# Performance work log

Hardware: AMD Instinct MI355X
Metric: run time of the kernel (lower is better)

The kernel has to match this reference:

```python
import jax, jax.numpy as jnp
import numpy as np

B, N, F_IN, H, S = 8, 2048, 128, 128, 2
ALPHA = 0.1  # LeakyReLU slope


def setup_inputs() -> dict:
    key = jax.random.key(0)
    ks = jax.random.split(key, 10)
    X_bt = jax.random.normal(ks[0], (B, N, F_IN), dtype=jnp.float32)
    distance_matrix = jax.random.uniform(ks[1], (N, N), dtype=jnp.float32)
    sigmas = jnp.array([0.2, 1.0], dtype=jnp.float32)  # GaussianKernelGenerator scales[:2]
    # Per-scale GeoGATLayer params (stacked on leading scale dim)
    W_w = jax.random.normal(ks[2], (S, H, F_IN), dtype=jnp.float32) * (1.0 / np.sqrt(F_IN))
    W_b = jnp.zeros((S, H), dtype=jnp.float32)
    # attn_fc: Linear(2H, 1) split into the two halves acting on h_i and h_j
    a_i = jax.random.normal(ks[3], (S, H), dtype=jnp.float32) * (1.0 / np.sqrt(2 * H))
    a_j = jax.random.normal(ks[4], (S, H), dtype=jnp.float32) * (1.0 / np.sqrt(2 * H))
    a_b = jnp.zeros((S,), dtype=jnp.float32)
    thr = jnp.full((S,), 0.3, dtype=jnp.float32)
    fus_w = jax.random.normal(ks[5], (H, S * H), dtype=jnp.float32) * (1.0 / np.sqrt(S * H))
    fus_b = jnp.zeros((H,), dtype=jnp.float32)
    return {"X_bt": X_bt, "distance_matrix": distance_matrix, "sigmas": sigmas,
            "W_w": W_w, "W_b": W_b, "a_i": a_i, "a_j": a_j, "a_b": a_b,
            "thr": thr, "fus_w": fus_w, "fus_b": fus_b}


def _leaky_relu(x):
    return jnp.where(x >= 0, x, ALPHA * x)


def reference(X_bt, distance_matrix, sigmas, W_w, W_b, a_i, a_j, a_b, thr, fus_w, fus_b):
    n = distance_matrix.shape[0]
    # layer clones dist and sets diag=1.0 (only for the 1/d additive bias)
    dist_diag1 = distance_matrix.at[jnp.diag_indices(n)].set(1.0)
    inv_d = 1.0 / (dist_diag1 + 1e-5)  # (N,N)
    outs = []
    for s in range(S):
        h = jnp.einsum('bnf,hf->bnh', X_bt, W_w[s]) + W_b[s]  # (B,N,H)
        # attn_fc(cat(h_i,h_j)) == h_i@a_i + h_j@a_j + bias (no concat materialized)
        si = h @ a_i[s]  # (B,N)
        sj = h @ a_j[s]  # (B,N)
        e = _leaky_relu(si[:, :, None] + sj[:, None, :] + a_b[s])  # (B,N,N)
        e = e + inv_d[None]
        A = jnp.exp(-distance_matrix ** 2 / (2.0 * sigmas[s] ** 2))  # Gaussian kernel
        mask = jax.nn.sigmoid(10.0 * (A - thr[s]))
        e = e * mask[None]
        attn = jax.nn.softmax(e, axis=-1)  # dropout is identity in eval
        outs.append(jnp.einsum('bnm,bmh->bnh', attn, h))
    H_cat = jnp.concatenate(outs, axis=-1)  # (B,N,S*H)
    return jnp.einsum('bnk,hk->bnh', H_cat, fus_w) + fus_b
```

## Files before the change

### kernel.cpp

```cpp
#include <hip/hip_runtime.h>
#include <cstdint>
#include <cstddef>

#define BB 8
#define NN 2048
#define FF 128
#define HH 128
#define SS 2
#define NT (NN / 64)

typedef _Float16 f16x8 __attribute__((ext_vector_type(8)));
typedef _Float16 f16x4 __attribute__((ext_vector_type(4)));
typedef float f32x4 __attribute__((ext_vector_type(4)));

__global__ __launch_bounds__(256) void geo_kernel(
    const float* __restrict__ dist, const float* __restrict__ sigmas,
    const float* __restrict__ thr, _Float16* __restrict__ g1, float* __restrict__ g2)
{
    const size_t idx = ((size_t)blockIdx.x * 256 + threadIdx.x) * 8;
    const int s = (int)(idx >> 22);
    const int i = (int)((idx >> 11) & (NN - 1));
    const int j0 = (int)(idx & (NN - 1));
    const float sg = sigmas[s];
    const float inv2s2 = 1.0f / (2.0f * sg * sg);
    const float th = thr[s];
    const float* dp = dist + (size_t)i * NN + j0;
    float4 d0 = *(const float4*)dp, d1 = *(const float4*)(dp + 4);
    float dv[8] = {d0.x, d0.y, d0.z, d0.w, d1.x, d1.y, d1.z, d1.w};
    f16x8 o1; float og[8];
    #pragma unroll
    for (int k = 0; k < 8; ++k) {
        float d = dv[k];
        float A = __expf(-d * d * inv2s2);
        float msk = 1.0f / (1.0f + __expf(-10.0f * (A - th)));
        float dd = (j0 + k == i) ? 1.0f : d;
        float invd = 1.0f / (dd + 1e-5f);
        o1[k] = (_Float16)msk;
        og[k] = msk * invd;
    }
    *(f16x8*)(g1 + idx) = o1;
    *(float4*)(g2 + idx)     = (float4){og[0], og[1], og[2], og[3]};
    *(float4*)(g2 + idx + 4) = (float4){og[4], og[5], og[6], og[7]};
}

__global__ __launch_bounds__(256, 2) void prep_kernel(
    const float* __restrict__ X, const float* __restrict__ Ww, const float* __restrict__ Wb,
    const float* __restrict__ ai, const float* __restrict__ aj, const float* __restrict__ ab,
    _Float16* __restrict__ h_t, float* __restrict__ srow, float* __restrict__ scol)
{
    const int s = blockIdx.z, b = blockIdx.y;
    const int n0 = blockIdx.x * 64;
    const int tid = threadIdx.x;
    __shared__ __align__(16) unsigned char smem[51200];
    float* sredI = (float*)(smem + 49152);
    float* sredJ = (float*)(smem + 49152 + 1024);

    {
        const int r = tid >> 2, fq = tid & 3;
        const float* src = X + ((size_t)b * NN + n0 + r) * FF + fq * 32;
        unsigned char* dst = smem + r * 256;
        const unsigned rs = r & 15;
        #pragma unroll
        for (int k = 0; k < 4; ++k) {
            float4 v0 = *(const float4*)(src + k * 8);
            float4 v1 = *(const float4*)(src + k * 8 + 4);
            f16x8 h;
            h[0]=(_Float16)v0.x; h[1]=(_Float16)v0.y; h[2]=(_Float16)v0.z; h[3]=(_Float16)v0.w;
            h[4]=(_Float16)v1.x; h[5]=(_Float16)v1.y; h[6]=(_Float16)v1.z; h[7]=(_Float16)v1.w;
            *(f16x8*)(dst + (((fq * 4 + k) ^ rs) << 4)) = h;
        }
    }
    {
        const int ch = tid >> 1, kh8 = (tid & 1) * 8;
        const float* src = Ww + ((size_t)s * HH + ch) * FF + kh8 * 8;
        unsigned char* dst = smem + 16384 + ch * 256;
        const unsigned cs = ch & 15;
        #pragma unroll
        for (int k = 0; k < 8; ++k) {
            float4 v0 = *(const float4*)(src + k * 8);
            float4 v1 = *(const float4*)(src + k * 8 + 4);
            f16x8 h;
            h[0]=(_Float16)v0.x; h[1]=(_Float16)v0.y; h[2]=(_Float16)v0.z; h[3]=(_Float16)v0.w;
            h[4]=(_Float16)v1.x; h[5]=(_Float16)v1.y; h[6]=(_Float16)v1.z; h[7]=(_Float16)v1.w;
            *(f16x8*)(dst + (((kh8 + k) ^ cs) << 4)) = h;
        }
    }
    __syncthreads();

    const int wave = tid >> 6, lane = tid & 63;
    const int lm = lane & 15, lq = lane >> 4;
    f32x4 acc[4][2];
    #pragma unroll
    for (int m = 0; m < 4; ++m)
        #pragma unroll
        for (int n = 0; n < 2; ++n) acc[m][n] = (f32x4){0.f, 0.f, 0.f, 0.f};

    #pragma unroll
    for (int ks = 0; ks < 4; ++ks) {
        f16x8 af[4], bf[2];
        #pragma unroll
        for (int m = 0; m < 4; ++m) {
            int r = m * 16 + lm;
            af[m] = *(const f16x8*)(smem + r * 256 + ((((ks << 2) | lq) ^ (r & 15)) << 4));
        }
        #pragma unroll
        for (int n = 0; n < 2; ++n) {
            int ch = wave * 32 + n * 16 + lm;
            bf[n] = *(const f16x8*)(smem + 16384 + ch * 256 + ((((ks << 2) | lq) ^ (ch & 15)) << 4));
        }
        #pragma unroll
        for (int m = 0; m < 4; ++m)
            #pragma unroll
            for (int n = 0; n < 2; ++n)
                acc[m][n] = __builtin_amdgcn_mfma_f32_16x16x32_f16(af[m], bf[n], acc[m][n], 0, 0, 0);
    }

    const float wb0 = Wb[s * HH + wave * 32 + lm];
    const float wb1 = Wb[s * HH + wave * 32 + 16 + lm];
    const float ai0 = ai[s * HH + wave * 32 + lm];
    const float ai1 = ai[s * HH + wave * 32 + 16 + lm];
    const float aj0 = aj[s * HH + wave * 32 + lm];
    const float aj1 = aj[s * HH + wave * 32 + 16 + lm];
    float pI[4][4], pJ[4][4];
    #pragma unroll
    for (int m = 0; m < 4; ++m) {
        #pragma unroll
        for (int r = 0; r < 4; ++r) {
            float h0 = acc[m][0][r] + wb0;
            float h1 = acc[m][1][r] + wb1;
            pI[m][r] = h0 * ai0 + h1 * ai1;
            pJ[m][r] = h0 * aj0 + h1 * aj1;
        }
        #pragma unroll
        for (int n = 0; n < 2; ++n) {
            float wb = n ? wb1 : wb0;
            f16x4 hv;
            #pragma unroll
            for (int r = 0; r < 4; ++r) hv[r] = (_Float16)(acc[m][n][r] + wb);
            int ch = wave * 32 + n * 16 + lm;
            *(f16x4*)(h_t + ((size_t)((s * BB + b) * HH + ch)) * NN + n0 + m * 16 + lq * 4) = hv;
        }
    }
    #pragma unroll
    for (int st = 1; st < 16; st <<= 1) {
        #pragma unroll
        for (int m = 0; m < 4; ++m)
            #pragma unroll
            for (int r = 0; r < 4; ++r) {
                pI[m][r] += __shfl_xor(pI[m][r], st);
                pJ[m][r] += __shfl_xor(pJ[m][r], st);
            }
    }
    if (lm == 0) {
        #pragma unroll
        for (int m = 0; m < 4; ++m)
            #pragma unroll
            for (int r = 0; r < 4; ++r) {
                sredI[wave * 64 + m * 16 + lq * 4 + r] = pI[m][r];
                sredJ[wave * 64 + m * 16 + lq * 4 + r] = pJ[m][r];
            }
    }
    __syncthreads();
    if (tid < 64) {
        float sI = sredI[tid] + sredI[64 + tid] + sredI[128 + tid] + sredI[192 + tid] + ab[s];
        float sJ = sredJ[tid] + sredJ[64 + tid] + sredJ[128 + tid] + sredJ[192 + tid];
        size_t idx = (size_t)(s * BB + b) * NN + n0 + tid;
        srow[idx] = sI;
        scol[idx] = sJ;
    }
}

template<bool GEO>
__global__ __launch_bounds__(256, 3) void attn_kernel(
    const float* __restrict__ dist, const float* __restrict__ sigmas,
    const float* __restrict__ thr, const _Float16* __restrict__ h_t,
    const float* __restrict__ srow, const float* __restrict__ scol,
    const _Float16* __restrict__ g1, const float* __restrict__ g2,
    _Float16* __restrict__ Hcat)
{
    const int s = blockIdx.z, b = blockIdx.y;
    const int i0 = blockIdx.x * 32;
    const int tid = threadIdx.x;

    __shared__ __align__(16) unsigned char smem[41344];
    float* scb    = (float*)(smem + 40960);
    float* lrow_s = (float*)(smem + 41216);

    const size_t sb = (size_t)(s * BB + b) * NN;
    const _Float16* hbase = h_t + (size_t)(s * BB + b) * HH * NN;

    const int wave = tid >> 6, lane = tid & 63;
    const int lm = lane & 15, lq = lane >> 4;
    const int chq = wave;

    const int row = tid >> 3, jg = tid & 7, jg8 = jg * 8;
    const int gi = i0 + row;
    const unsigned rsw = row & 7;
    const float si = srow[sb + gi];
    const size_t girow = ((size_t)s * NN + gi) * NN;
    const size_t drow = (size_t)gi * NN;

    const int sch = tid >> 1, shf4 = (tid & 1) * 4;
    const _Float16* hrow = hbase + (size_t)sch * NN + (shf4 >> 2) * 32;
    const unsigned hsw = sch & 7;

    float inv2s2 = 0.f, th = 0.f;
    if (!GEO) { float sg = sigmas[s]; inv2s2 = 1.0f / (2.0f * sg * sg); th = thr[s]; }

    f32x4 acc[2][2];
    #pragma unroll
    for (int m = 0; m < 2; ++m)
        #pragma unroll
        for (int n = 0; n < 2; ++n) acc[m][n] = (f32x4){0.f, 0.f, 0.f, 0.f};
    float m_r = -3.0e38f, l_r = 0.f;

    f16x8 hA[4], hB[4], gA, gB;
    f32x4 qA[2], qB[2];

#define LOADT(HT, GT, QT, J0V) {                                              \
    const _Float16* hp_ = hrow + (J0V);                                       \
    HT[0] = *(const f16x8*)(hp_);                                             \
    HT[1] = *(const f16x8*)(hp_ + 8);                                         \
    HT[2] = *(const f16x8*)(hp_ + 16);                                        \
    HT[3] = *(const f16x8*)(hp_ + 24);                                        \
    const int jb_ = (J0V) + jg8;                                              \
    if (GEO) {                                                                \
        GT = *(const f16x8*)(g1 + girow + jb_);                               \
        QT[0] = *(const f32x4*)(g2 + girow + jb_);                            \
        QT[1] = *(const f32x4*)(g2 + girow + jb_ + 4);                        \
    } else {                                                                  \
        (void)GT;                                                             \
        QT[0] = *(const f32x4*)(dist + drow + jb_);                           \
        QT[1] = *(const f32x4*)(dist + drow + jb_ + 4);                       \
    }                                                                         \
}

#define MFMA_STEP(MB) {                                                       \
    f16x8 af00, af01, af10, af11, bf00, bf01, bf10, bf11;                     \
    { const unsigned char* pb_ = smem + (MB) * 4096;                          \
      int r_ = lm; unsigned sw_ = r_ & 7;                                     \
      af00 = *(const f16x8*)(pb_ + r_ * 128 + ((lq ^ sw_) << 4));             \
      af01 = *(const f16x8*)(pb_ + r_ * 128 + (((4 | lq) ^ sw_) << 4));       \
      r_ = 16 + lm; sw_ = r_ & 7;                                             \
      af10 = *(const f16x8*)(pb_ + r_ * 128 + ((lq ^ sw_) << 4));             \
      af11 = *(const f16x8*)(pb_ + r_ * 128 + (((4 | lq) ^ sw_) << 4)); }     \
    { const unsigned char* hb_ = smem + 8192 + (MB) * 16384;                  \
      int c_ = chq * 32 + lm; unsigned sw_ = c_ & 7;                          \
      bf00 = *(const f16x8*)(hb_ + c_ * 128 + ((lq ^ sw_) << 4));             \
      bf01 = *(const f16x8*)(hb_ + c_ * 128 + (((4 | lq) ^ sw_) << 4));       \
      c_ = chq * 32 + 16 + lm; sw_ = c_ & 7;                                  \
      bf10 = *(const f16x8*)(hb_ + c_ * 128 + ((lq ^ sw_) << 4));             \
      bf11 = *(const f16x8*)(hb_ + c_ * 128 + (((4 | lq) ^ sw_) << 4)); }     \
    f32x4 sc0 = *(const f32x4*)(scb + (MB) * 32 + lq * 4);                    \
    f32x4 sc1 = *(const f32x4*)(scb + (MB) * 32 + 16 + lq * 4);               \
    acc[0][0] *= sc0; acc[0][1] *= sc0;                                       \
    acc[1][0] *= sc1; acc[1][1] *= sc1;                                       \
    acc[0][0] = __builtin_amdgcn_mfma_f32_16x16x32_f16(af00, bf00, acc[0][0], 0, 0, 0); \
    acc[0][0] = __builtin_amdgcn_mfma_f32_16x16x32_f16(af01, bf01, acc[0][0], 0, 0, 0); \
    acc[0][1] = __builtin_amdgcn_mfma_f32_16x16x32_f16(af00, bf10, acc[0][1], 0, 0, 0); \
    acc[0][1] = __builtin_amdgcn_mfma_f32_16x16x32_f16(af01, bf11, acc[0][1], 0, 0, 0); \
    acc[1][0] = __builtin_amdgcn_mfma_f32_16x16x32_f16(af10, bf00, acc[1][0], 0, 0, 0); \
    acc[1][0] = __builtin_amdgcn_mfma_f32_16x16x32_f16(af11, bf01, acc[1][0], 0, 0, 0); \
    acc[1][1] = __builtin_amdgcn_mfma_f32_16x16x32_f16(af10, bf10, acc[1][1], 0, 0, 0); \
    acc[1][1] = __builtin_amdgcn_mfma_f32_16x16x32_f16(af11, bf11, acc[1][1], 0, 0, 0); \
}

#define PHASE1(HC, GC, QC, J0, PB) {                                          \
    unsigned char* hd_ = smem + 8192 + (PB) * 16384 + sch * 128;              \
    *(f16x8*)(hd_ + (((shf4 + 0) ^ hsw) << 4)) = HC[0];                       \
    *(f16x8*)(hd_ + (((shf4 + 1) ^ hsw) << 4)) = HC[1];                       \
    *(f16x8*)(hd_ + (((shf4 + 2) ^ hsw) << 4)) = HC[2];                       \
    *(f16x8*)(hd_ + (((shf4 + 3) ^ hsw) << 4)) = HC[3];                       \
    const int jb_ = (J0) + jg8;                                               \
    f32x4 c0_ = *(const f32x4*)(scol + sb + jb_);                             \
    f32x4 c1_ = *(const f32x4*)(scol + sb + jb_ + 4);                         \
    float ev[8];                                                              \
    if (GEO) {                                                                \
        _Pragma("unroll")                                                     \
        for (int k = 0; k < 8; ++k) {                                         \
            float t_ = si + (k < 4 ? c0_[k & 3] : c1_[k & 3]);                \
            float lr_ = fmaxf(t_, 0.1f * t_);                                 \
            ev[k] = fmaf(lr_, (float)GC[k], QC[k >> 2][k & 3]);               \
        }                                                                     \
    } else {                                                                  \
        _Pragma("unroll")                                                     \
        for (int k = 0; k < 8; ++k) {                                         \
            float d_ = QC[k >> 2][k & 3];                                     \
            float A_ = __expf(-d_ * d_ * inv2s2);                             \
            float den_ = 1.0f + __expf(-10.0f * (A_ - th));                   \
            float r1_ = __builtin_amdgcn_rcpf(den_); r1_ = r1_ * (2.0f - den_ * r1_); \
            float dd_ = (jb_ + k == gi) ? 1.0f : d_;                          \
            float x2_ = dd_ + 1e-5f;                                          \
            float ri_ = __builtin_amdgcn_rcpf(x2_); ri_ = ri_ * (2.0f - x2_ * ri_);   \
            float t_ = si + (k < 4 ? c0_[k & 3] : c1_[k & 3]);                \
            float lr_ = fmaxf(t_, 0.1f * t_);                                 \
            ev[k] = (lr_ + ri_) * r1_;                                        \
        }                                                                     \
    }                                                                         \
    float mt_ = fmaxf(fmaxf(fmaxf(ev[0], ev[1]), fmaxf(ev[2], ev[3])),        \
                      fmaxf(fmaxf(ev[4], ev[5]), fmaxf(ev[6], ev[7])));       \
    mt_ = fmaxf(mt_, __shfl_xor(mt_, 1));                                     \
    mt_ = fmaxf(mt_, __shfl_xor(mt_, 2));                                     \
    mt_ = fmaxf(mt_, __shfl_xor(mt_, 4));                                     \
    const float mnew_ = fmaxf(m_r, mt_);                                      \
    float ps_ = 0.f; f16x8 pv_;                                               \
    _Pragma("unroll")                                                         \
    for (int k = 0; k < 8; ++k) {                                             \
        float p_ = __expf(ev[k] - mnew_);                                     \
        ps_ += p_; pv_[k] = (_Float16)p_;                                     \
    }                                                                         \
    ps_ += __shfl_xor(ps_, 1);                                                \
    ps_ += __shfl_xor(ps_, 2);                                                \
    ps_ += __shfl_xor(ps_, 4);                                                \
    *(f16x8*)(smem + (PB) * 4096 + row * 128 + ((jg ^ rsw) << 4)) = pv_;      \
    float scl_ = __expf(m_r - mnew_);                                         \
    if (jg == 0) scb[(PB) * 32 + row] = scl_;                                 \
    l_r = l_r * scl_ + ps_;                                                   \
    m_r = mnew_;                                                              \
}

#define WINDOW(HC, GC, QC, HN, GN, QN, JT, PB, MB) {                          \
    int jn_ = (JT) + 1; if (jn_ >= NT) jn_ = 0;                               \
    LOADT(HN, GN, QN, jn_ * 64);                                              \
    if ((JT) > 0) MFMA_STEP(MB);                                              \
    PHASE1(HC, GC, QC, (JT) * 64, PB);                                        \
    __syncthreads();                                                          \
}

    LOADT(hA, gA, qA, 0);
    for (int jt = 0; jt < NT; jt += 2) {
        WINDOW(hA, gA, qA, hB, gB, qB, jt,     0, 1);
        WINDOW(hB, gB, qB, hA, gA, qA, jt + 1, 1, 0);
    }
    if (jg == 0) lrow_s[row] = l_r;
    MFMA_STEP(1);
    __syncthreads();

    _Float16* ebuf = (_Float16*)smem;
    #pragma unroll
    for (int m = 0; m < 2; ++m) {
        f32x4 lv = *(const f32x4*)&lrow_s[m * 16 + lq * 4];
        f32x4 inv;
        #pragma unroll
        for (int r = 0; r < 4; ++r) {
            float x = lv[r];
            float iv = __builtin_amdgcn_rcpf(x);
            inv[r] = iv * (2.0f - x * iv);
        }
        #pragma unroll
        for (int n = 0; n < 2; ++n)
            #pragma unroll
            for (int r = 0; r < 4; ++r)
                ebuf[(m * 16 + lq * 4 + r) * 128 + chq * 32 + n * 16 + lm] =
                    (_Float16)(acc[m][n][r] * inv[r]);
    }
    __syncthreads();
    {
        const int r = tid >> 3, c0 = (tid & 7) * 16;
        f16x8 v0 = *(const f16x8*)(ebuf + r * 128 + c0);
        f16x8 v1 = *(const f16x8*)(ebuf + r * 128 + c0 + 8);
        _Float16* dst = Hcat + ((size_t)(b * NN + i0 + r)) * (SS * HH) + s * HH + c0;
        *(f16x8*)dst = v0;
        *(f16x8*)(dst + 8) = v1;
    }
#undef LOADT
#undef MFMA_STEP
#undef PHASE1
#undef WINDOW
}

__global__ __launch_bounds__(256, 2) void fuse_kernel(
    const _Float16* __restrict__ Hcat, const float* __restrict__ fw,
    const float* __restrict__ fb, float* __restrict__ out)
{
    const int r0 = blockIdx.x * 32;
    const int tid = threadIdx.x;
    __shared__ __align__(16) unsigned char smem[49152];

    {
        const int r = tid >> 3, q = tid & 7;
        const _Float16* src = Hcat + (size_t)(r0 + r) * 256 + q * 32;
        unsigned char* dst = smem + r * 512;
        const unsigned rs = r & 7;
        #pragma unroll
        for (int k = 0; k < 4; ++k) {
            f16x8 v = *(const f16x8*)(src + k * 8);
            *(f16x8*)(dst + (((q * 4 + k) ^ rs) << 4)) = v;
        }
    }

    const int wave = tid >> 6, lane = tid & 63;
    const int lm = lane & 15, lq = lane >> 4;
    f32x4 acc[2][2];
    #pragma unroll
    for (int m = 0; m < 2; ++m)
        #pragma unroll
        for (int n = 0; n < 2; ++n) acc[m][n] = (f32x4){0.f, 0.f, 0.f, 0.f};

    for (int c = 0; c < 2; ++c) {
        __syncthreads();
        {
            const int ch = tid >> 1, kh8 = (tid & 1) * 8;
            const float* src = fw + (size_t)ch * 256 + c * 128 + kh8 * 8;
            unsigned char* dst = smem + 16384 + ch * 256;
            const unsigned cs = ch & 15;
            #pragma unroll
            for (int k = 0; k < 8; ++k) {
                float4 v0 = *(const float4*)(src + k * 8);
                float4 v1 = *(const float4*)(src + k * 8 + 4);
                f16x8 h;
                h[0]=(_Float16)v0.x; h[1]=(_Float16)v0.y; h[2]=(_Float16)v0.z; h[3]=(_Float16)v0.w;
                h[4]=(_Float16)v1.x; h[5]=(_Float16)v1.y; h[6]=(_Float16)v1.z; h[7]=(_Float16)v1.w;
                *(f16x8*)(dst + (((kh8 + k) ^ cs) << 4)) = h;
            }
        }
        __syncthreads();
        #pragma unroll
        for (int ks = 0; ks < 4; ++ks) {
            const int gks = c * 4 + ks;
            f16x8 af[2], bf[2];
            #pragma unroll
            for (int m = 0; m < 2; ++m) {
                int r = m * 16 + lm;
                af[m] = *(const f16x8*)(smem + r * 512 + ((((gks << 2) | lq) ^ (r & 7)) << 4));
            }
            #pragma unroll
            for (int n = 0; n < 2; ++n) {
                int ch = wave * 32 + n * 16 + lm;
                bf[n] = *(const f16x8*)(smem + 16384 + ch * 256 + ((((ks << 2) | lq) ^ (ch & 15)) << 4));
            }
            #pragma unroll
            for (int m = 0; m < 2; ++m)
                #pragma unroll
                for (int n = 0; n < 2; ++n)
                    acc[m][n] = __builtin_amdgcn_mfma_f32_16x16x32_f16(af[m], bf[n], acc[m][n], 0, 0, 0);
        }
    }
    {
        float fb0 = fb[wave * 32 + lm];
        float fb1 = fb[wave * 32 + 16 + lm];
        #pragma unroll
        for (int m = 0; m < 2; ++m)
            #pragma unroll
            for (int n = 0; n < 2; ++n) {
                float fbv = n ? fb1 : fb0;
                int ch = wave * 32 + n * 16 + lm;
                #pragma unroll
                for (int r = 0; r < 4; ++r)
                    out[(size_t)(r0 + m * 16 + lq * 4 + r) * HH + ch] = acc[m][n][r] + fbv;
            }
    }
}

extern "C" void kernel_launch(void* const* d_in, const int* in_sizes, int n_in,
                              void* d_out, int out_size, void* d_ws, size_t ws_size,
                              hipStream_t stream)
{
    const float* X      = (const float*)d_in[0];
    const float* dist   = (const float*)d_in[1];
    const float* sigmas = (const float*)d_in[2];
    const float* Ww     = (const float*)d_in[3];
    const float* Wb     = (const float*)d_in[4];
    const float* ai     = (const float*)d_in[5];
    const float* aj     = (const float*)d_in[6];
    const float* ab     = (const float*)d_in[7];
    const float* thr    = (const float*)d_in[8];
    const float* fw     = (const float*)d_in[9];
    const float* fb     = (const float*)d_in[10];
    float* out = (float*)d_out;

    char* ws = (char*)d_ws;
    float*     srow = (float*)(ws);
    float*     scol = (float*)(ws + 131072);
    _Float16*  h_t  = (_Float16*)(ws + 262144);
    _Float16*  Hcat = (_Float16*)(ws + 8650752);
    _Float16*  g1   = (_Float16*)(ws + 17039360);
    float*     g2   = (float*)(ws + 33816576);
    const bool geo = ws_size >= (size_t)67371008;

    prep_kernel<<<dim3(NN / 64, BB, SS), 256, 0, stream>>>(X, Ww, Wb, ai, aj, ab, h_t, srow, scol);
    if (geo) {
        geo_kernel<<<(SS * NN * NN / 8) / 256, 256, 0, stream>>>(dist, sigmas, thr, g1, g2);
        attn_kernel<true><<<dim3(NN / 32, BB, SS), 256, 0, stream>>>(
            dist, sigmas, thr, h_t, srow, scol, g1, g2, Hcat);
    } else {
        attn_kernel<false><<<dim3(NN / 32, BB, SS), 256, 0, stream>>>(
            dist, sigmas, thr, h_t, srow, scol, (const _Float16*)nullptr, (const float*)nullptr, Hcat);
    }
    fuse_kernel<<<BB * NN / 32, 256, 0, stream>>>(Hcat, fw, fb, out);
}
```

Measured before the change: 193.9 us.

## Compute geo mask inline in attention, sharing it across two batches per block

```diff
diff --git a/kernel.cpp b/kernel.cpp
--- a/kernel.cpp
+++ b/kernel.cpp
@@ -12,36 +12,6 @@
 typedef _Float16 f16x8 __attribute__((ext_vector_type(8)));
 typedef _Float16 f16x4 __attribute__((ext_vector_type(4)));
 typedef float f32x4 __attribute__((ext_vector_type(4)));
-
-__global__ __launch_bounds__(256) void geo_kernel(
-    const float* __restrict__ dist, const float* __restrict__ sigmas,
-    const float* __restrict__ thr, _Float16* __restrict__ g1, float* __restrict__ g2)
-{
-    const size_t idx = ((size_t)blockIdx.x * 256 + threadIdx.x) * 8;
-    const int s = (int)(idx >> 22);
-    const int i = (int)((idx >> 11) & (NN - 1));
-    const int j0 = (int)(idx & (NN - 1));
-    const float sg = sigmas[s];
-    const float inv2s2 = 1.0f / (2.0f * sg * sg);
-    const float th = thr[s];
-    const float* dp = dist + (size_t)i * NN + j0;
-    float4 d0 = *(const float4*)dp, d1 = *(const float4*)(dp + 4);
-    float dv[8] = {d0.x, d0.y, d0.z, d0.w, d1.x, d1.y, d1.z, d1.w};
-    f16x8 o1; float og[8];
-    #pragma unroll
-    for (int k = 0; k < 8; ++k) {
-        float d = dv[k];
-        float A = __expf(-d * d * inv2s2);
-        float msk = 1.0f / (1.0f + __expf(-10.0f * (A - th)));
-        float dd = (j0 + k == i) ? 1.0f : d;
-        float invd = 1.0f / (dd + 1e-5f);
-        o1[k] = (_Float16)msk;
-        og[k] = msk * invd;
-    }
-    *(f16x8*)(g1 + idx) = o1;
-    *(float4*)(g2 + idx)     = (float4){og[0], og[1], og[2], og[3]};
-    *(float4*)(g2 + idx + 4) = (float4){og[4], og[5], og[6], og[7]};
-}
 
 __global__ __launch_bounds__(256, 2) void prep_kernel(
     const float* __restrict__ X, const float* __restrict__ Ww, const float* __restrict__ Wb,
@@ -123,7 +93,7 @@
     const float aj1 = aj[s * HH + wave * 32 + 16 + lm];
     float pI[4][4], pJ[4][4];
     #pragma unroll
-    for (int m = 0; m < 4; ++m) {
+    for (int m = 0; m < 4; ++m)
         #pragma unroll
         for (int r = 0; r < 4; ++r) {
             float h0 = acc[m][0][r] + wb0;
@@ -131,16 +101,6 @@
             pI[m][r] = h0 * ai0 + h1 * ai1;
             pJ[m][r] = h0 * aj0 + h1 * aj1;
         }
-        #pragma unroll
-        for (int n = 0; n < 2; ++n) {
-            float wb = n ? wb1 : wb0;
-            f16x4 hv;
-            #pragma unroll
-            for (int r = 0; r < 4; ++r) hv[r] = (_Float16)(acc[m][n][r] + wb);
-            int ch = wave * 32 + n * 16 + lm;
-            *(f16x4*)(h_t + ((size_t)((s * BB + b) * HH + ch)) * NN + n0 + m * 16 + lq * 4) = hv;
-        }
-    }
     #pragma unroll
     for (int st = 1; st < 16; st <<= 1) {
         #pragma unroll
@@ -151,6 +111,22 @@
                 pJ[m][r] += __shfl_xor(pJ[m][r], st);
             }
     }
+    __syncthreads();
+
+    {
+        #pragma unroll
+        for (int m = 0; m < 4; ++m)
+            #pragma unroll
+            for (int n = 0; n < 2; ++n) {
+                float wb = n ? wb1 : wb0;
+                f16x4 hv;
+                #pragma unroll
+                for (int r = 0; r < 4; ++r) hv[r] = (_Float16)(acc[m][n][r] + wb);
+                int ch = wave * 32 + n * 16 + lm;
+                int slot = m * 2 + (lq >> 1);
+                *(f16x4*)(smem + ch * 128 + ((slot ^ (ch & 7)) << 4) + (lq & 1) * 8) = hv;
+            }
+    }
     if (lm == 0) {
         #pragma unroll
         for (int m = 0; m < 4; ++m)
@@ -161,6 +137,16 @@
             }
     }
     __syncthreads();
+    {
+        const int ch = tid >> 1, half = tid & 1;
+        _Float16* dst = h_t + ((size_t)((s * BB + b) * HH + ch)) * NN + n0 + half * 32;
+        const unsigned cs = ch & 7;
+        #pragma unroll
+        for (int k = 0; k < 4; ++k) {
+            f16x8 v = *(const f16x8*)(smem + ch * 128 + (((half * 4 + k) ^ cs) << 4));
+            *(f16x8*)(dst + k * 8) = v;
+        }
+    }
     if (tid < 64) {
         float sI = sredI[tid] + sredI[64 + tid] + sredI[128 + tid] + sredI[192 + tid] + ab[s];
         float sJ = sredJ[tid] + sredJ[64 + tid] + sredJ[128 + tid] + sredJ[192 + tid];
@@ -170,203 +156,181 @@
     }
 }
 
-template<bool GEO>
-__global__ __launch_bounds__(256, 3) void attn_kernel(
+__global__ __launch_bounds__(512, 4) void attn_kernel(
     const float* __restrict__ dist, const float* __restrict__ sigmas,
     const float* __restrict__ thr, const _Float16* __restrict__ h_t,
     const float* __restrict__ srow, const float* __restrict__ scol,
-    const _Float16* __restrict__ g1, const float* __restrict__ g2,
     _Float16* __restrict__ Hcat)
 {
-    const int s = blockIdx.z, b = blockIdx.y;
-    const int i0 = blockIdx.x * 32;
+    const int bx = blockIdx.x;
+    const int grp = bx & 7;
+    const int i0 = (bx >> 3) * 32;
+    const int s = grp >> 2;
+    const int b0 = (grp & 3) * 2;
+
+    __shared__ __align__(16) unsigned char smem[41472];
+    float* scb  = (float*)(smem + 40960);
+    float* lrow = (float*)(smem + 41216);
+
     const int tid = threadIdx.x;
-
-    __shared__ __align__(16) unsigned char smem[41344];
-    float* scb    = (float*)(smem + 40960);
-    float* lrow_s = (float*)(smem + 41216);
-
-    const size_t sb = (size_t)(s * BB + b) * NN;
-    const _Float16* hbase = h_t + (size_t)(s * BB + b) * HH * NN;
-
     const int wave = tid >> 6, lane = tid & 63;
     const int lm = lane & 15, lq = lane >> 4;
-    const int chq = wave;
-
-    const int row = tid >> 3, jg = tid & 7, jg8 = jg * 8;
+
+    const float sg = sigmas[s];
+    const float inv2s2 = 1.0f / (2.0f * sg * sg);
+    const float th = thr[s];
+
+    const int row = tid >> 4, jq = tid & 15;
     const int gi = i0 + row;
-    const unsigned rsw = row & 7;
-    const float si = srow[sb + gi];
-    const size_t girow = ((size_t)s * NN + gi) * NN;
-    const size_t drow = (size_t)gi * NN;
-
-    const int sch = tid >> 1, shf4 = (tid & 1) * 4;
-    const _Float16* hrow = hbase + (size_t)sch * NN + (shf4 >> 2) * 32;
+    const size_t sb0 = (size_t)(s * BB + b0) * NN;
+    const size_t sb1 = sb0 + NN;
+    const float si0 = srow[sb0 + gi];
+    const float si1 = srow[sb1 + gi];
+    const float* drow = dist + (size_t)gi * NN;
+
+    const int sch = tid >> 2, sq = tid & 3;
+    const _Float16* hb0 = h_t + ((size_t)((s * BB + b0) * HH + sch)) * NN;
+    const _Float16* hb1 = hb0 + (size_t)HH * NN;
+    unsigned char* hd0 = smem + 8192 + sch * 128;
+    unsigned char* hd1 = hd0 + 16384;
     const unsigned hsw = sch & 7;
 
-    float inv2s2 = 0.f, th = 0.f;
-    if (!GEO) { float sg = sigmas[s]; inv2s2 = 1.0f / (2.0f * sg * sg); th = thr[s]; }
+    const int wb = wave >> 2, cq = wave & 3;
 
     f32x4 acc[2][2];
     #pragma unroll
     for (int m = 0; m < 2; ++m)
         #pragma unroll
         for (int n = 0; n < 2; ++n) acc[m][n] = (f32x4){0.f, 0.f, 0.f, 0.f};
-    float m_r = -3.0e38f, l_r = 0.f;
-
-    f16x8 hA[4], hB[4], gA, gB;
-    f32x4 qA[2], qB[2];
-
-#define LOADT(HT, GT, QT, J0V) {                                              \
-    const _Float16* hp_ = hrow + (J0V);                                       \
-    HT[0] = *(const f16x8*)(hp_);                                             \
-    HT[1] = *(const f16x8*)(hp_ + 8);                                         \
-    HT[2] = *(const f16x8*)(hp_ + 16);                                        \
-    HT[3] = *(const f16x8*)(hp_ + 24);                                        \
-    const int jb_ = (J0V) + jg8;                                              \
-    if (GEO) {                                                                \
-        GT = *(const f16x8*)(g1 + girow + jb_);                               \
-        QT[0] = *(const f32x4*)(g2 + girow + jb_);                            \
-        QT[1] = *(const f32x4*)(g2 + girow + jb_ + 4);                        \
-    } else {                                                                  \
-        (void)GT;                                                             \
-        QT[0] = *(const f32x4*)(dist + drow + jb_);                           \
-        QT[1] = *(const f32x4*)(dist + drow + jb_ + 4);                       \
-    }                                                                         \
-}
-
-#define MFMA_STEP(MB) {                                                       \
-    f16x8 af00, af01, af10, af11, bf00, bf01, bf10, bf11;                     \
-    { const unsigned char* pb_ = smem + (MB) * 4096;                          \
-      int r_ = lm; unsigned sw_ = r_ & 7;                                     \
-      af00 = *(const f16x8*)(pb_ + r_ * 128 + ((lq ^ sw_) << 4));             \
-      af01 = *(const f16x8*)(pb_ + r_ * 128 + (((4 | lq) ^ sw_) << 4));       \
-      r_ = 16 + lm; sw_ = r_ & 7;                                             \
-      af10 = *(const f16x8*)(pb_ + r_ * 128 + ((lq ^ sw_) << 4));             \
-      af11 = *(const f16x8*)(pb_ + r_ * 128 + (((4 | lq) ^ sw_) << 4)); }     \
-    { const unsigned char* hb_ = smem + 8192 + (MB) * 16384;                  \
-      int c_ = chq * 32 + lm; unsigned sw_ = c_ & 7;                          \
-      bf00 = *(const f16x8*)(hb_ + c_ * 128 + ((lq ^ sw_) << 4));             \
-      bf01 = *(const f16x8*)(hb_ + c_ * 128 + (((4 | lq) ^ sw_) << 4));       \
-      c_ = chq * 32 + 16 + lm; sw_ = c_ & 7;                                  \
-      bf10 = *(const f16x8*)(hb_ + c_ * 128 + ((lq ^ sw_) << 4));             \
-      bf11 = *(const f16x8*)(hb_ + c_ * 128 + (((4 | lq) ^ sw_) << 4)); }     \
-    f32x4 sc0 = *(const f32x4*)(scb + (MB) * 32 + lq * 4);                    \
-    f32x4 sc1 = *(const f32x4*)(scb + (MB) * 32 + 16 + lq * 4);               \
-    acc[0][0] *= sc0; acc[0][1] *= sc0;                                       \
-    acc[1][0] *= sc1; acc[1][1] *= sc1;                                       \
-    acc[0][0] = __builtin_amdgcn_mfma_f32_16x16x32_f16(af00, bf00, acc[0][0], 0, 0, 0); \
-    acc[0][0] = __builtin_amdgcn_mfma_f32_16x16x32_f16(af01, bf01, acc[0][0], 0, 0, 0); \
-    acc[0][1] = __builtin_amdgcn_mfma_f32_16x16x32_f16(af00, bf10, acc[0][1], 0, 0, 0); \
-    acc[0][1] = __builtin_amdgcn_mfma_f32_16x16x32_f16(af01, bf11, acc[0][1], 0, 0, 0); \
-    acc[1][0] = __builtin_amdgcn_mfma_f32_16x16x32_f16(af10, bf00, acc[1][0], 0, 0, 0); \
-    acc[1][0] = __builtin_amdgcn_mfma_f32_16x16x32_f16(af11, bf01, acc[1][0], 0, 0, 0); \
-    acc[1][1] = __builtin_amdgcn_mfma_f32_16x16x32_f16(af10, bf10, acc[1][1], 0, 0, 0); \
-    acc[1][1] = __builtin_amdgcn_mfma_f32_16x16x32_f16(af11, bf11, acc[1][1], 0, 0, 0); \
-}
-
-#define PHASE1(HC, GC, QC, J0, PB) {                                          \
-    unsigned char* hd_ = smem + 8192 + (PB) * 16384 + sch * 128;              \
-    *(f16x8*)(hd_ + (((shf4 + 0) ^ hsw) << 4)) = HC[0];                       \
-    *(f16x8*)(hd_ + (((shf4 + 1) ^ hsw) << 4)) = HC[1];                       \
-    *(f16x8*)(hd_ + (((shf4 + 2) ^ hsw) << 4)) = HC[2];                       \
-    *(f16x8*)(hd_ + (((shf4 + 3) ^ hsw) << 4)) = HC[3];                       \
-    const int jb_ = (J0) + jg8;                                               \
-    f32x4 c0_ = *(const f32x4*)(scol + sb + jb_);                             \
-    f32x4 c1_ = *(const f32x4*)(scol + sb + jb_ + 4);                         \
-    float ev[8];                                                              \
-    if (GEO) {                                                                \
-        _Pragma("unroll")                                                     \
-        for (int k = 0; k < 8; ++k) {                                         \
-            float t_ = si + (k < 4 ? c0_[k & 3] : c1_[k & 3]);                \
-            float lr_ = fmaxf(t_, 0.1f * t_);                                 \
-            ev[k] = fmaf(lr_, (float)GC[k], QC[k >> 2][k & 3]);               \
-        }                                                                     \
-    } else {                                                                  \
-        _Pragma("unroll")                                                     \
-        for (int k = 0; k < 8; ++k) {                                         \
-            float d_ = QC[k >> 2][k & 3];                                     \
-            float A_ = __expf(-d_ * d_ * inv2s2);                             \
-            float den_ = 1.0f + __expf(-10.0f * (A_ - th));                   \
-            float r1_ = __builtin_amdgcn_rcpf(den_); r1_ = r1_ * (2.0f - den_ * r1_); \
-            float dd_ = (jb_ + k == gi) ? 1.0f : d_;                          \
-            float x2_ = dd_ + 1e-5f;                                          \
-            float ri_ = __builtin_amdgcn_rcpf(x2_); ri_ = ri_ * (2.0f - x2_ * ri_);   \
-            float t_ = si + (k < 4 ? c0_[k & 3] : c1_[k & 3]);                \
-            float lr_ = fmaxf(t_, 0.1f * t_);                                 \
-            ev[k] = (lr_ + ri_) * r1_;                                        \
-        }                                                                     \
-    }                                                                         \
-    float mt_ = fmaxf(fmaxf(fmaxf(ev[0], ev[1]), fmaxf(ev[2], ev[3])),        \
-                      fmaxf(fmaxf(ev[4], ev[5]), fmaxf(ev[6], ev[7])));       \
-    mt_ = fmaxf(mt_, __shfl_xor(mt_, 1));                                     \
-    mt_ = fmaxf(mt_, __shfl_xor(mt_, 2));                                     \
-    mt_ = fmaxf(mt_, __shfl_xor(mt_, 4));                                     \
-    const float mnew_ = fmaxf(m_r, mt_);                                      \
-    float ps_ = 0.f; f16x8 pv_;                                               \
-    _Pragma("unroll")                                                         \
-    for (int k = 0; k < 8; ++k) {                                             \
-        float p_ = __expf(ev[k] - mnew_);                                     \
-        ps_ += p_; pv_[k] = (_Float16)p_;                                     \
-    }                                                                         \
-    ps_ += __shfl_xor(ps_, 1);                                                \
-    ps_ += __shfl_xor(ps_, 2);                                                \
-    ps_ += __shfl_xor(ps_, 4);                                                \
-    *(f16x8*)(smem + (PB) * 4096 + row * 128 + ((jg ^ rsw) << 4)) = pv_;      \
-    float scl_ = __expf(m_r - mnew_);                                         \
-    if (jg == 0) scb[(PB) * 32 + row] = scl_;                                 \
-    l_r = l_r * scl_ + ps_;                                                   \
-    m_r = mnew_;                                                              \
-}
-
-#define WINDOW(HC, GC, QC, HN, GN, QN, JT, PB, MB) {                          \
-    int jn_ = (JT) + 1; if (jn_ >= NT) jn_ = 0;                               \
-    LOADT(HN, GN, QN, jn_ * 64);                                              \
-    if ((JT) > 0) MFMA_STEP(MB);                                              \
-    PHASE1(HC, GC, QC, (JT) * 64, PB);                                        \
-    __syncthreads();                                                          \
-}
-
-    LOADT(hA, gA, qA, 0);
-    for (int jt = 0; jt < NT; jt += 2) {
-        WINDOW(hA, gA, qA, hB, gB, qB, jt,     0, 1);
-        WINDOW(hB, gB, qB, hA, gA, qA, jt + 1, 1, 0);
-    }
-    if (jg == 0) lrow_s[row] = l_r;
-    MFMA_STEP(1);
+    float m0 = -3.0e38f, m1 = -3.0e38f, l0 = 0.f, l1 = 0.f;
+
+    for (int jt = 0; jt < NT; ++jt) {
+        const int j0 = jt * 64;
+        f16x8 hv00 = *(const f16x8*)(hb0 + j0 + sq * 8);
+        f16x8 hv01 = *(const f16x8*)(hb0 + j0 + 32 + sq * 8);
+        f16x8 hv10 = *(const f16x8*)(hb1 + j0 + sq * 8);
+        f16x8 hv11 = *(const f16x8*)(hb1 + j0 + 32 + sq * 8);
+
+        const int jb = j0 + jq * 4;
+        f32x4 dv = *(const f32x4*)(drow + jb);
+        f32x4 c0 = *(const f32x4*)(scol + sb0 + jb);
+        f32x4 c1 = *(const f32x4*)(scol + sb1 + jb);
+        float e0[4], e1[4];
+        #pragma unroll
+        for (int k = 0; k < 4; ++k) {
+            float d = dv[k];
+            float A = __expf(-d * d * inv2s2);
+            float den = 1.0f + __expf(-10.0f * (A - th));
+            float msk = __builtin_amdgcn_rcpf(den);
+            float dd = (jb + k == gi) ? 1.0f : d;
+            float x2 = dd + 1e-5f;
+            float ri = __builtin_amdgcn_rcpf(x2);
+            ri = ri * (2.0f - x2 * ri);
+            float t0 = si0 + c0[k]; t0 = fmaxf(t0, 0.1f * t0);
+            float t1 = si1 + c1[k]; t1 = fmaxf(t1, 0.1f * t1);
+            e0[k] = (t0 + ri) * msk;
+            e1[k] = (t1 + ri) * msk;
+        }
+        float mt0 = fmaxf(fmaxf(e0[0], e0[1]), fmaxf(e0[2], e0[3]));
+        float mt1 = fmaxf(fmaxf(e1[0], e1[1]), fmaxf(e1[2], e1[3]));
+        #pragma unroll
+        for (int st = 1; st < 16; st <<= 1) {
+            mt0 = fmaxf(mt0, __shfl_xor(mt0, st));
+            mt1 = fmaxf(mt1, __shfl_xor(mt1, st));
+        }
+        const float mn0 = fmaxf(m0, mt0), mn1 = fmaxf(m1, mt1);
+        f16x4 pv0, pv1;
+        float ps0 = 0.f, ps1 = 0.f;
+        #pragma unroll
+        for (int k = 0; k < 4; ++k) {
+            float p0 = __expf(e0[k] - mn0); ps0 += p0; pv0[k] = (_Float16)p0;
+            float p1 = __expf(e1[k] - mn1); ps1 += p1; pv1[k] = (_Float16)p1;
+        }
+        #pragma unroll
+        for (int st = 1; st < 16; st <<= 1) {
+            ps0 += __shfl_xor(ps0, st);
+            ps1 += __shfl_xor(ps1, st);
+        }
+        {
+            const unsigned off = row * 128 + (((jq >> 1) ^ (row & 7)) << 4) + (jq & 1) * 8;
+            *(f16x4*)(smem + off) = pv0;
+            *(f16x4*)(smem + 4096 + off) = pv1;
+        }
+        float scl0 = __expf(m0 - mn0), scl1 = __expf(m1 - mn1);
+        l0 = l0 * scl0 + ps0; m0 = mn0;
+        l1 = l1 * scl1 + ps1; m1 = mn1;
+        if (jq == 0) { scb[row] = scl0; scb[32 + row] = scl1; }
+
+        *(f16x8*)(hd0 + ((sq ^ hsw) << 4)) = hv00;
+        *(f16x8*)(hd0 + (((sq + 4) ^ hsw) << 4)) = hv01;
+        *(f16x8*)(hd1 + ((sq ^ hsw) << 4)) = hv10;
+        *(f16x8*)(hd1 + (((sq + 4) ^ hsw) << 4)) = hv11;
+        __syncthreads();
+
+        {
+            const unsigned char* Pb = smem + wb * 4096;
+            const unsigned char* Hb = smem + 8192 + wb * 16384;
+            const int ra = lm;           const unsigned sa = ra & 7;
+            const int rb = 16 + lm;      const unsigned sbw = rb & 7;
+            f16x8 a00 = *(const f16x8*)(Pb + ra * 128 + ((lq ^ sa) << 4));
+            f16x8 a01 = *(const f16x8*)(Pb + ra * 128 + (((4 | lq) ^ sa) << 4));
+            f16x8 a10 = *(const f16x8*)(Pb + rb * 128 + ((lq ^ sbw) << 4));
+            f16x8 a11 = *(const f16x8*)(Pb + rb * 128 + (((4 | lq) ^ sbw) << 4));
+            const int ca = cq * 32 + lm;      const unsigned ta = ca & 7;
+            const int cb = cq * 32 + 16 + lm; const unsigned tb = cb & 7;
+            f16x8 b00 = *(const f16x8*)(Hb + ca * 128 + ((lq ^ ta) << 4));
+            f16x8 b01 = *(const f16x8*)(Hb + ca * 128 + (((4 | lq) ^ ta) << 4));
+            f16x8 b10 = *(const f16x8*)(Hb + cb * 128 + ((lq ^ tb) << 4));
+            f16x8 b11 = *(const f16x8*)(Hb + cb * 128 + (((4 | lq) ^ tb) << 4));
+            f32x4 sA = *(const f32x4*)(scb + wb * 32 + lq * 4);
+            f32x4 sB = *(const f32x4*)(scb + wb * 32 + 16 + lq * 4);
+            acc[0][0] *= sA; acc[0][1] *= sA;
+            acc[1][0] *= sB; acc[1][1] *= sB;
+            acc[0][0] = __builtin_amdgcn_mfma_f32_16x16x32_f16(a00, b00, acc[0][0], 0, 0, 0);
+            acc[0][0] = __builtin_amdgcn_mfma_f32_16x16x32_f16(a01, b01, acc[0][0], 0, 0, 0);
+            acc[0][1] = __builtin_amdgcn_mfma_f32_16x16x32_f16(a00, b10, acc[0][1], 0, 0, 0);
+            acc[0][1] = __builtin_amdgcn_mfma_f32_16x16x32_f16(a01, b11, acc[0][1], 0, 0, 0);
+            acc[1][0] = __builtin_amdgcn_mfma_f32_16x16x32_f16(a10, b00, acc[1][0], 0, 0, 0);
+            acc[1][0] = __builtin_amdgcn_mfma_f32_16x16x32_f16(a11, b01, acc[1][0], 0, 0, 0);
+            acc[1][1] = __builtin_amdgcn_mfma_f32_16x16x32_f16(a10, b10, acc[1][1], 0, 0, 0);
+            acc[1][1] = __builtin_amdgcn_mfma_f32_16x16x32_f16(a11, b11, acc[1][1], 0, 0, 0);
+        }
+        __syncthreads();
+    }
+
+    if (jq == 0) { lrow[row] = l0; lrow[32 + row] = l1; }
     __syncthreads();
 
     _Float16* ebuf = (_Float16*)smem;
-    #pragma unroll
-    for (int m = 0; m < 2; ++m) {
-        f32x4 lv = *(const f32x4*)&lrow_s[m * 16 + lq * 4];
-        f32x4 inv;
+    {
+        f32x4 lvA = *(const f32x4*)(lrow + wb * 32 + lq * 4);
+        f32x4 lvB = *(const f32x4*)(lrow + wb * 32 + 16 + lq * 4);
+        f32x4 iA, iB;
         #pragma unroll
         for (int r = 0; r < 4; ++r) {
-            float x = lv[r];
-            float iv = __builtin_amdgcn_rcpf(x);
-            inv[r] = iv * (2.0f - x * iv);
-        }
-        #pragma unroll
-        for (int n = 0; n < 2; ++n)
-            #pragma unroll
-            for (int r = 0; r < 4; ++r)
-                ebuf[(m * 16 + lq * 4 + r) * 128 + chq * 32 + n * 16 + lm] =
-                    (_Float16)(acc[m][n][r] * inv[r]);
+            float xa = lvA[r], xb = lvB[r];
+            float va = __builtin_amdgcn_rcpf(xa); iA[r] = va * (2.0f - xa * va);
+            float vb = __builtin_amdgcn_rcpf(xb); iB[r] = vb * (2.0f - xb * vb);
+        }
+        #pragma unroll
+        for (int m = 0; m < 2; ++m)
+            #pragma unroll
+            for (int n = 0; n < 2; ++n)
+                #pragma unroll
+                for (int r = 0; r < 4; ++r) {
+                    float inv = m ? iB[r] : iA[r];
+                    ebuf[wb * 4096 + (m * 16 + lq * 4 + r) * 128 + cq * 32 + n * 16 + lm] =
+                        (_Float16)(acc[m][n][r] * inv);
+                }
     }
     __syncthreads();
-    {
-        const int r = tid >> 3, c0 = (tid & 7) * 16;
-        f16x8 v0 = *(const f16x8*)(ebuf + r * 128 + c0);
-        f16x8 v1 = *(const f16x8*)(ebuf + r * 128 + c0 + 8);
-        _Float16* dst = Hcat + ((size_t)(b * NN + i0 + r)) * (SS * HH) + s * HH + c0;
-        *(f16x8*)dst = v0;
-        *(f16x8*)(dst + 8) = v1;
-    }
-#undef LOADT
-#undef MFMA_STEP
-#undef PHASE1
-#undef WINDOW
+    #pragma unroll
+    for (int rep = 0; rep < 2; ++rep) {
+        const int idx = tid + rep * 512;
+        const int eb = idx >> 9, erow = (idx >> 4) & 31, u = idx & 15;
+        f16x8 v = *(const f16x8*)(ebuf + eb * 4096 + erow * 128 + u * 8);
+        *(f16x8*)(Hcat + ((size_t)((b0 + eb) * NN + i0 + erow)) * (SS * HH) + s * HH + u * 8) = v;
+    }
 }
 
 __global__ __launch_bounds__(256, 2) void fuse_kernel(
@@ -464,9 +428,9 @@
     const float* ai     = (const float*)d_in[5];
     const float* aj     = (const float*)d_in[6];
     const float* ab     = (const float*)d_in[7];
-    const float* thr    = (const float*)d_in[8];
     const float* fw     = (const float*)d_in[9];
     const float* fb     = (const float*)d_in[10];
+    const float* thr    = (const float*)d_in[8];
     float* out = (float*)d_out;
 
     char* ws = (char*)d_ws;
@@ -474,18 +438,8 @@
     float*     scol = (float*)(ws + 131072);
     _Float16*  h_t  = (_Float16*)(ws + 262144);
     _Float16*  Hcat = (_Float16*)(ws + 8650752);
-    _Float16*  g1   = (_Float16*)(ws + 17039360);
-    float*     g2   = (float*)(ws + 33816576);
-    const bool geo = ws_size >= (size_t)67371008;
 
     prep_kernel<<<dim3(NN / 64, BB, SS), 256, 0, stream>>>(X, Ww, Wb, ai, aj, ab, h_t, srow, scol);
-    if (geo) {
-        geo_kernel<<<(SS * NN * NN / 8) / 256, 256, 0, stream>>>(dist, sigmas, thr, g1, g2);
-        attn_kernel<true><<<dim3(NN / 32, BB, SS), 256, 0, stream>>>(
-            dist, sigmas, thr, h_t, srow, scol, g1, g2, Hcat);
-    } else {
-        attn_kernel<false><<<dim3(NN / 32, BB, SS), 256, 0, stream>>>(
-            dist, sigmas, thr, h_t, srow, scol, (const _Float16*)nullptr, (const float*)nullptr, Hcat);
-    }
+    attn_kernel<<<512, 512, 0, stream>>>(dist, sigmas, thr, h_t, srow, scol, Hcat);
     fuse_kernel<<<BB * NN / 32, 256, 0, stream>>>(Hcat, fw, fb, out);
 }
```

Measured after the change: 190.3 us. No clear change (-1.9%).
